# Kernel tuning notes

Hardware: AMD Instinct MI355X
Metric: run time of the kernel (lower is better)

## Reference

```python
import jax, jax.numpy as jnp
import numpy as np

D = 768
HEAD_SIZE = 64  # D / num_heads = 768 / 12

def setup_inputs() -> dict:
    key = jax.random.key(0)
    k1, k2, k3, k4 = jax.random.split(key, 4)
    ix = jax.random.normal(k1, (8, 4096, D), dtype=jnp.float32)
    # Linear(D, head_size, bias=False) weights; stored as [D, head_size] for x @ W
    scale = 1.0 / np.sqrt(D)
    Wk = jax.random.uniform(k2, (D, HEAD_SIZE), dtype=jnp.float32, minval=-scale, maxval=scale)
    Wq = jax.random.uniform(k3, (D, HEAD_SIZE), dtype=jnp.float32, minval=-scale, maxval=scale)
    Wv = jax.random.uniform(k4, (D, HEAD_SIZE), dtype=jnp.float32, minval=-scale, maxval=scale)
    return {"ix": ix, "Wk": Wk, "Wq": Wq, "Wv": Wv}

def reference(ix, Wk, Wq, Wv):
    # ix: [B, S, D]
    k = ix @ Wk  # [B, S, H]
    q = ix @ Wq  # [B, S, H]
    v = ix @ Wv  # [B, S, H]
    scale = 1.0 / jnp.sqrt(jnp.asarray(HEAD_SIZE, ix.dtype))
    wei = jnp.einsum('bsh,bth->bst', q, k) * scale  # [B, S, S]
    wei = jax.nn.softmax(wei, axis=-1)
    out = jnp.einsum('bst,bth->bsh', wei, v)  # [B, S, H]
    return out
```

## Files before the change

kernel.cpp:

```cpp
#include <hip/hip_runtime.h>
#include <hip/hip_bf16.h>

#define D_DIM 768
#define HS 64
#define SEQ 4096
#define NBATCH 8

typedef short bf8 __attribute__((ext_vector_type(8)));
typedef short bf4 __attribute__((ext_vector_type(4)));
typedef float f4 __attribute__((ext_vector_type(4)));

static __device__ __forceinline__ short f2b(float x) {
    __hip_bfloat16 h = __float2bfloat16(x);
    return __builtin_bit_cast(short, h);
}
static __device__ __forceinline__ unsigned pk2(float x, float y) {
    unsigned ux = __builtin_bit_cast(unsigned, x) + 0x8000u;
    unsigned uy = __builtin_bit_cast(unsigned, y) + 0x8000u;
    return __builtin_amdgcn_perm(uy, ux, 0x07060302u);
}

#if defined(__has_builtin)
#if __has_builtin(__builtin_amdgcn_exp2f)
#define EXP2F(x) __builtin_amdgcn_exp2f(x)
#endif
#endif
#ifndef EXP2F
#define EXP2F(x) exp2f(x)
#endif

__global__ __launch_bounds__(256) void wconv_kernel(
    const float* __restrict__ Wk, const float* __restrict__ Wq,
    const float* __restrict__ Wv, short* __restrict__ wt3)
{
    int tid = blockIdx.x * 256 + threadIdx.x;
    int mat = tid / (D_DIM * HS);
    int rem = tid - mat * (D_DIM * HS);
    int k = rem >> 6;
    int n = rem & 63;
    const float* W = (mat == 0) ? Wk : (mat == 1) ? Wq : Wv;
    float scale = (mat == 1) ? 0.18033688011112042f : 1.0f;
    int cc = mat * HS + n;
    int c = k >> 5, q = (k >> 3) & 3, e = k & 7;
    wt3[(c * 192 + cc) * 32 + q * 8 + e] = f2b(W[rem] * scale);
}

__global__ __launch_bounds__(256, 3) void proj_kernel(
    const float* __restrict__ ix, const short* __restrict__ wt3,
    short* __restrict__ qg, short* __restrict__ kg, short* __restrict__ vg)
{
    __shared__ short ixl[2][32 * 72];

    const int t = threadIdx.x;
    const int wave = t >> 6, lane = t & 63;
    const int m = lane & 15, quad = lane >> 4;
    const int m0 = blockIdx.x * 32;

    const int srow = t >> 3;
    const int skoff = (t & 7) * 8;

    f4 xr0, xr1;
    auto load_ix = [&](int c) {
        const float* px = ix + (m0 + srow) * D_DIM + c * 64 + skoff;
        xr0 = *(const f4*)px;
        xr1 = *(const f4*)(px + 4);
    };
    auto write_ix = [&](int p) {
        uint4 xw;
        xw.x = pk2(xr0[0], xr0[1]);
        xw.y = pk2(xr0[2], xr0[3]);
        xw.z = pk2(xr1[0], xr1[1]);
        xw.w = pk2(xr1[2], xr1[3]);
        *(uint4*)(&ixl[p][srow * 72 + skoff]) = xw;
    };

    const int colb = wave * 48;
    const short* wbase = wt3 + (colb + m) * 32 + quad * 8;

    bf8 wb[2][2][3];
    auto load_w = [&](int c, int buf) {
        #pragma unroll
        for (int nt = 0; nt < 3; ++nt) {
            const short* pw = wbase + ((size_t)(2 * c) * 192 + nt * 16) * 32;
            wb[buf][0][nt] = *(const bf8*)pw;
            wb[buf][1][nt] = *(const bf8*)(pw + 192 * 32);
        }
    };

    f4 acc[2][3] = {};

    load_ix(0); load_w(0, 0); write_ix(0); __syncthreads();

    #pragma unroll
    for (int c = 0; c < 12; ++c) {
        const int p = c & 1;
        if (c + 1 < 12) { load_ix(c + 1); load_w(c + 1, (c + 1) & 1); }

        bf8 a0 = *(const bf8*)(&ixl[p][m * 72 + quad * 8]);
        bf8 a1 = *(const bf8*)(&ixl[p][m * 72 + 32 + quad * 8]);
        bf8 a2 = *(const bf8*)(&ixl[p][(16 + m) * 72 + quad * 8]);
        bf8 a3 = *(const bf8*)(&ixl[p][(16 + m) * 72 + 32 + quad * 8]);

        #pragma unroll
        for (int nt = 0; nt < 3; ++nt) {
            acc[0][nt] = __builtin_amdgcn_mfma_f32_16x16x32_bf16(a0, wb[p][0][nt], acc[0][nt], 0, 0, 0);
            acc[0][nt] = __builtin_amdgcn_mfma_f32_16x16x32_bf16(a1, wb[p][1][nt], acc[0][nt], 0, 0, 0);
            acc[1][nt] = __builtin_amdgcn_mfma_f32_16x16x32_bf16(a2, wb[p][0][nt], acc[1][nt], 0, 0, 0);
            acc[1][nt] = __builtin_amdgcn_mfma_f32_16x16x32_bf16(a3, wb[p][1][nt], acc[1][nt], 0, 0, 0);
        }

        if (c + 1 < 12) { write_ix((c + 1) & 1); __syncthreads(); }
    }

    #pragma unroll
    for (int mt = 0; mt < 2; ++mt) {
        const int row = m0 + mt * 16 + quad * 4;
        #pragma unroll
        for (int nt = 0; nt < 3; ++nt) {
            const int cb = colb + nt * 16;
            short* op = (cb < 64) ? kg : (cb < 128) ? qg : vg;
            const int n = (cb & 63) + m;
            #pragma unroll
            for (int r = 0; r < 4; ++r)
                op[(row + r) * HS + n] = f2b(acc[mt][nt][r]);
        }
    }
}

__global__ __launch_bounds__(256, 2) void attn_kernel(
    const short* __restrict__ qg, const short* __restrict__ kg,
    const short* __restrict__ vg, float* __restrict__ num0,
    float* __restrict__ num1, float* __restrict__ num2,
    float* __restrict__ num3, float* __restrict__ den0,
    float* __restrict__ den1, float* __restrict__ den2,
    float* __restrict__ den3)
{
    __shared__ short kl[2][64 * 72];
    __shared__ short vl[2][64 * 64];

    const int t = threadIdx.x;
    const int wave = t >> 6, lane = t & 63;
    const int m = lane & 15, quad = lane >> 4;

    const int flat = blockIdx.x;
    const int lg = (flat & 7) * 64 + (flat >> 3);
    const int qx = lg & 15;
    const int ks = (lg >> 4) & 3;
    const int b  = lg >> 6;

    const int rbase = b * SEQ;
    const int kbase = rbase + ks * (SEQ / 4);
    const int qw = qx * 256 + wave * 64;

    float* __restrict__ nump = (ks == 0) ? num0 : (ks == 1) ? num1 : (ks == 2) ? num2 : num3;
    float* __restrict__ denp = (ks == 0) ? den0 : (ks == 1) ? den1 : (ks == 2) ? den2 : den3;

    bf8 qf[4][2];
    #pragma unroll
    for (int nq = 0; nq < 4; ++nq)
        #pragma unroll
        for (int st = 0; st < 2; ++st)
            qf[nq][st] = *(const bf8*)(qg + (rbase + qw + nq * 16 + m) * HS + st * 32 + quad * 8);

    bf8 ones;
    #pragma unroll
    for (int i = 0; i < 8; ++i) ones[i] = (short)0x3F80;

    const int srow = t >> 2, soff = (t & 3) * 16;
    const int jp = t >> 3, dg = t & 7;
    const int j0 = jp * 2;
    const int jj = j0 & 31;
    const int gj = j0 >> 5;
    const int vq = (jj >> 2) & 3;
    const int vh = (jj >> 4) & 1;
    const int vb = (jj & 3) >> 1;
    const int vcol_base = vh * 4 + 2 * vb;
    const int vchunk_l = 4 * gj + vq;

    uint4 kr0, kr1, vr0, vr1;
    auto load_chunk = [&](int c) {
        const short* pk = kg + (kbase + c * 64 + srow) * HS + soff;
        kr0 = *(const uint4*)pk; kr1 = *(const uint4*)(pk + 8);
        const short* pv = vg + (kbase + c * 64 + j0) * HS + dg * 8;
        vr0 = *(const uint4*)pv; vr1 = *(const uint4*)(pv + HS);
    };
    auto write_chunk = [&](int p) {
        *(bf8*)(&kl[p][srow * 72 + soff])     = __builtin_bit_cast(bf8, kr0);
        *(bf8*)(&kl[p][srow * 72 + soff + 8]) = __builtin_bit_cast(bf8, kr1);
        bf8 v0 = __builtin_bit_cast(bf8, vr0), v1 = __builtin_bit_cast(bf8, vr1);
        #pragma unroll
        for (int i = 0; i < 8; ++i) {
            const int d = dg * 8 + i;
            const int chunk = vchunk_l ^ (i ^ dg);
            unsigned val = (unsigned short)v0[i] | ((unsigned)(unsigned short)v1[i] << 16);
            *(unsigned*)(&vl[p][d * 64 + chunk * 8 + vcol_base]) = val;
        }
    };

    f4 o[4][4] = {};
    f4 dacc[4] = {};

    load_chunk(0); write_chunk(0); __syncthreads();

    const int NCH = SEQ / 4 / 64;
    for (int c = 0; c < NCH; ++c) {
        const int p = c & 1;
        if (c + 1 < NCH) load_chunk(c + 1);

        __builtin_amdgcn_s_setprio(1);
        #pragma unroll
        for (int g = 0; g < 2; ++g) {
            bf8 kA0 = *(const bf8*)(&kl[p][(g * 32 + m) * 72 + quad * 8]);
            bf8 kA1 = *(const bf8*)(&kl[p][(g * 32 + m) * 72 + 32 + quad * 8]);
            bf8 kB0 = *(const bf8*)(&kl[p][(g * 32 + 16 + m) * 72 + quad * 8]);
            bf8 kB1 = *(const bf8*)(&kl[p][(g * 32 + 16 + m) * 72 + 32 + quad * 8]);

            bf8 vf[4];
            #pragma unroll
            for (int dt = 0; dt < 4; ++dt) {
                const int row = dt * 16 + m;
                const int key = (m & 7) ^ (2 * dt + (m >> 3));
                const int chunk = (g * 4 + quad) ^ key;
                vf[dt] = *(const bf8*)(&vl[p][row * 64 + chunk * 8]);
            }

            #pragma unroll
            for (int nq = 0; nq < 4; ++nq) {
                f4 sa = {0.f, 0.f, 0.f, 0.f}, sb = {0.f, 0.f, 0.f, 0.f};
                sa = __builtin_amdgcn_mfma_f32_16x16x32_bf16(kA0, qf[nq][0], sa, 0, 0, 0);
                sa = __builtin_amdgcn_mfma_f32_16x16x32_bf16(kA1, qf[nq][1], sa, 0, 0, 0);
                sb = __builtin_amdgcn_mfma_f32_16x16x32_bf16(kB0, qf[nq][0], sb, 0, 0, 0);
                sb = __builtin_amdgcn_mfma_f32_16x16x32_bf16(kB1, qf[nq][1], sb, 0, 0, 0);
                float e0 = EXP2F(sa[0]), e1 = EXP2F(sa[1]), e2 = EXP2F(sa[2]), e3 = EXP2F(sa[3]);
                float e4 = EXP2F(sb[0]), e5 = EXP2F(sb[1]), e6 = EXP2F(sb[2]), e7 = EXP2F(sb[3]);
                uint4 pu;
                pu.x = pk2(e0, e1); pu.y = pk2(e2, e3);
                pu.z = pk2(e4, e5); pu.w = pk2(e6, e7);
                bf8 pf = __builtin_bit_cast(bf8, pu);
                dacc[nq] = __builtin_amdgcn_mfma_f32_16x16x32_bf16(ones, pf, dacc[nq], 0, 0, 0);
                #pragma unroll
                for (int dt = 0; dt < 4; ++dt)
                    o[nq][dt] = __builtin_amdgcn_mfma_f32_16x16x32_bf16(vf[dt], pf, o[nq][dt], 0, 0, 0);
            }
        }
        __builtin_amdgcn_s_setprio(0);

        if (c + 1 < NCH) { write_chunk((c + 1) & 1); __syncthreads(); }
    }

    #pragma unroll
    for (int nq = 0; nq < 4; ++nq) {
        const int orow = rbase + qw + nq * 16 + m;
        if (quad == 0) denp[orow] = dacc[nq][0];
        #pragma unroll
        for (int dt = 0; dt < 4; ++dt)
            *(f4*)(nump + orow * HS + dt * 16 + quad * 4) = o[nq][dt];
    }
}

__global__ __launch_bounds__(256) void reduce_kernel(
    float* __restrict__ out, const float* __restrict__ num1,
    const float* __restrict__ num2, const float* __restrict__ num3,
    const float* __restrict__ den0, const float* __restrict__ den1,
    const float* __restrict__ den2, const float* __restrict__ den3)
{
    const int gid = blockIdx.x * 256 + threadIdx.x;
    const int base = gid * 4;
    const int r = base >> 6;
    f4 n0 = *(const f4*)(out + base);
    f4 n1 = *(const f4*)(num1 + base);
    f4 n2 = *(const f4*)(num2 + base);
    f4 n3 = *(const f4*)(num3 + base);
    const float rs = 1.0f / ((den0[r] + den1[r]) + (den2[r] + den3[r]));
    f4 res;
    #pragma unroll
    for (int i = 0; i < 4; ++i) res[i] = ((n0[i] + n1[i]) + (n2[i] + n3[i])) * rs;
    *(f4*)(out + base) = res;
}

extern "C" void kernel_launch(void* const* d_in, const int* in_sizes, int n_in,
                              void* d_out, int out_size, void* d_ws, size_t ws_size,
                              hipStream_t stream) {
    const float* ix = (const float*)d_in[0];
    const float* Wk = (const float*)d_in[1];
    const float* Wq = (const float*)d_in[2];
    const float* Wv = (const float*)d_in[3];
    float* out = (float*)d_out;

    const size_t NQKV = (size_t)NBATCH * SEQ * HS;
    short* qg = (short*)d_ws;
    short* kg = qg + NQKV;
    short* vg = kg + NQKV;
    short* wt3 = vg + NQKV;
    char*  fbase = (char*)(wt3 + 24 * 192 * 32);
    float* num1 = (float*)fbase;
    float* num2 = num1 + NQKV;
    float* num3 = num2 + NQKV;
    float* den0 = num3 + NQKV;
    float* den1 = den0 + (size_t)NBATCH * SEQ;
    float* den2 = den1 + (size_t)NBATCH * SEQ;
    float* den3 = den2 + (size_t)NBATCH * SEQ;

    wconv_kernel<<<(3 * D_DIM * HS) / 256, 256, 0, stream>>>(Wk, Wq, Wv, wt3);
    proj_kernel<<<(NBATCH * SEQ) / 32, 256, 0, stream>>>(ix, wt3, qg, kg, vg);
    attn_kernel<<<512, 256, 0, stream>>>(qg, kg, vg, out, num1, num2, num3,
                                         den0, den1, den2, den3);
    reduce_kernel<<<(int)(NQKV / (256 * 4)), 256, 0, stream>>>(
        out, num1, num2, num3, den0, den1, den2, den3);
}
```

Before: 217.3 us.

## Deepen prefetch to two chunks ahead in projection and attention kernels

Both the projection and attention kernels now keep two register sets of staged global loads, so chunk c+2 is fetched while chunk c is computed. The loop is unrolled by two to alternate register sets. In the attention kernel the LDS write of the next chunk is moved between the two compute halves to overlap it with MFMA work. The aim is to hide more global-load latency, at the cost of extra VGPRs, which may reduce occupancy or cause spills under the launch bounds.

```diff
diff --git a/kernel.cpp b/kernel.cpp
--- a/kernel.cpp
+++ b/kernel.cpp
@@ -59,18 +59,18 @@
     const int srow = t >> 3;
     const int skoff = (t & 7) * 8;
 
-    f4 xr0, xr1;
-    auto load_ix = [&](int c) {
+    f4 xa0, xa1, xb0, xb1;
+    auto load_ix = [&](int c, f4& r0, f4& r1) {
         const float* px = ix + (m0 + srow) * D_DIM + c * 64 + skoff;
-        xr0 = *(const f4*)px;
-        xr1 = *(const f4*)(px + 4);
-    };
-    auto write_ix = [&](int p) {
+        r0 = *(const f4*)px;
+        r1 = *(const f4*)(px + 4);
+    };
+    auto write_ix = [&](int p, f4 r0, f4 r1) {
         uint4 xw;
-        xw.x = pk2(xr0[0], xr0[1]);
-        xw.y = pk2(xr0[2], xr0[3]);
-        xw.z = pk2(xr1[0], xr1[1]);
-        xw.w = pk2(xr1[2], xr1[3]);
+        xw.x = pk2(r0[0], r0[1]);
+        xw.y = pk2(r0[2], r0[3]);
+        xw.z = pk2(r1[0], r1[1]);
+        xw.w = pk2(r1[2], r1[3]);
         *(uint4*)(&ixl[p][srow * 72 + skoff]) = xw;
     };
 
@@ -89,18 +89,18 @@
 
     f4 acc[2][3] = {};
 
-    load_ix(0); load_w(0, 0); write_ix(0); __syncthreads();
-
-    #pragma unroll
-    for (int c = 0; c < 12; ++c) {
-        const int p = c & 1;
-        if (c + 1 < 12) { load_ix(c + 1); load_w(c + 1, (c + 1) & 1); }
-
+    load_ix(0, xa0, xa1);
+    load_w(0, 0);
+    write_ix(0, xa0, xa1);
+    load_ix(1, xb0, xb1);
+    load_w(1, 1);
+    __syncthreads();
+
+    auto mfma_block = [&](int p) {
         bf8 a0 = *(const bf8*)(&ixl[p][m * 72 + quad * 8]);
         bf8 a1 = *(const bf8*)(&ixl[p][m * 72 + 32 + quad * 8]);
         bf8 a2 = *(const bf8*)(&ixl[p][(16 + m) * 72 + quad * 8]);
         bf8 a3 = *(const bf8*)(&ixl[p][(16 + m) * 72 + 32 + quad * 8]);
-
         #pragma unroll
         for (int nt = 0; nt < 3; ++nt) {
             acc[0][nt] = __builtin_amdgcn_mfma_f32_16x16x32_bf16(a0, wb[p][0][nt], acc[0][nt], 0, 0, 0);
@@ -108,8 +108,23 @@
             acc[1][nt] = __builtin_amdgcn_mfma_f32_16x16x32_bf16(a2, wb[p][0][nt], acc[1][nt], 0, 0, 0);
             acc[1][nt] = __builtin_amdgcn_mfma_f32_16x16x32_bf16(a3, wb[p][1][nt], acc[1][nt], 0, 0, 0);
         }
-
-        if (c + 1 < 12) { write_ix((c + 1) & 1); __syncthreads(); }
+    };
+
+    for (int cc = 0; cc < 12; cc += 2) {
+        {
+            const int c = cc;
+            if (c + 2 < 12) load_ix(c + 2, xa0, xa1);
+            mfma_block(0);
+            if (c + 2 < 12) load_w(c + 2, 0);
+            if (c + 1 < 12) { write_ix(1, xb0, xb1); __syncthreads(); }
+        }
+        {
+            const int c = cc + 1;
+            if (c + 2 < 12) load_ix(c + 2, xb0, xb1);
+            mfma_block(1);
+            if (c + 2 < 12) load_w(c + 2, 1);
+            if (c + 1 < 12) { write_ix(0, xa0, xa1); __syncthreads(); }
+        }
     }
 
     #pragma unroll
@@ -155,17 +170,6 @@
     float* __restrict__ nump = (ks == 0) ? num0 : (ks == 1) ? num1 : (ks == 2) ? num2 : num3;
     float* __restrict__ denp = (ks == 0) ? den0 : (ks == 1) ? den1 : (ks == 2) ? den2 : den3;
 
-    bf8 qf[4][2];
-    #pragma unroll
-    for (int nq = 0; nq < 4; ++nq)
-        #pragma unroll
-        for (int st = 0; st < 2; ++st)
-            qf[nq][st] = *(const bf8*)(qg + (rbase + qw + nq * 16 + m) * HS + st * 32 + quad * 8);
-
-    bf8 ones;
-    #pragma unroll
-    for (int i = 0; i < 8; ++i) ones[i] = (short)0x3F80;
-
     const int srow = t >> 2, soff = (t & 3) * 16;
     const int jp = t >> 3, dg = t & 7;
     const int j0 = jp * 2;
@@ -177,17 +181,18 @@
     const int vcol_base = vh * 4 + 2 * vb;
     const int vchunk_l = 4 * gj + vq;
 
-    uint4 kr0, kr1, vr0, vr1;
-    auto load_chunk = [&](int c) {
+    uint4 kA0r, kA1r, vA0r, vA1r;
+    uint4 kB0r, kB1r, vB0r, vB1r;
+    auto load_chunk = [&](int c, uint4& k0, uint4& k1, uint4& v0, uint4& v1) {
         const short* pk = kg + (kbase + c * 64 + srow) * HS + soff;
-        kr0 = *(const uint4*)pk; kr1 = *(const uint4*)(pk + 8);
+        k0 = *(const uint4*)pk; k1 = *(const uint4*)(pk + 8);
         const short* pv = vg + (kbase + c * 64 + j0) * HS + dg * 8;
-        vr0 = *(const uint4*)pv; vr1 = *(const uint4*)(pv + HS);
-    };
-    auto write_chunk = [&](int p) {
-        *(bf8*)(&kl[p][srow * 72 + soff])     = __builtin_bit_cast(bf8, kr0);
-        *(bf8*)(&kl[p][srow * 72 + soff + 8]) = __builtin_bit_cast(bf8, kr1);
-        bf8 v0 = __builtin_bit_cast(bf8, vr0), v1 = __builtin_bit_cast(bf8, vr1);
+        v0 = *(const uint4*)pv; v1 = *(const uint4*)(pv + HS);
+    };
+    auto write_chunk = [&](int p, uint4 k0, uint4 k1, uint4 v0r, uint4 v1r) {
+        *(bf8*)(&kl[p][srow * 72 + soff])     = __builtin_bit_cast(bf8, k0);
+        *(bf8*)(&kl[p][srow * 72 + soff + 8]) = __builtin_bit_cast(bf8, k1);
+        bf8 v0 = __builtin_bit_cast(bf8, v0r), v1 = __builtin_bit_cast(bf8, v1r);
         #pragma unroll
         for (int i = 0; i < 8; ++i) {
             const int d = dg * 8 + i;
@@ -200,52 +205,84 @@
     f4 o[4][4] = {};
     f4 dacc[4] = {};
 
-    load_chunk(0); write_chunk(0); __syncthreads();
+    bf8 ones;
+    #pragma unroll
+    for (int i = 0; i < 8; ++i) ones[i] = (short)0x3F80;
+
+    load_chunk(0, kA0r, kA1r, vA0r, vA1r);
+
+    bf8 qf[4][2];
+    #pragma unroll
+    for (int nq = 0; nq < 4; ++nq)
+        #pragma unroll
+        for (int st = 0; st < 2; ++st)
+            qf[nq][st] = *(const bf8*)(qg + (rbase + qw + nq * 16 + m) * HS + st * 32 + quad * 8);
+
+    write_chunk(0, kA0r, kA1r, vA0r, vA1r);
+    load_chunk(1, kB0r, kB1r, vB0r, vB1r);
+    __syncthreads();
+
+    auto compute_g = [&](int p, int g) {
+        bf8 kA0 = *(const bf8*)(&kl[p][(g * 32 + m) * 72 + quad * 8]);
+        bf8 kA1 = *(const bf8*)(&kl[p][(g * 32 + m) * 72 + 32 + quad * 8]);
+        bf8 kB0 = *(const bf8*)(&kl[p][(g * 32 + 16 + m) * 72 + quad * 8]);
+        bf8 kB1 = *(const bf8*)(&kl[p][(g * 32 + 16 + m) * 72 + 32 + quad * 8]);
+
+        bf8 vf[4];
+        #pragma unroll
+        for (int dt = 0; dt < 4; ++dt) {
+            const int row = dt * 16 + m;
+            const int key = (m & 7) ^ (2 * dt + (m >> 3));
+            const int chunk = (g * 4 + quad) ^ key;
+            vf[dt] = *(const bf8*)(&vl[p][row * 64 + chunk * 8]);
+        }
+
+        #pragma unroll
+        for (int nq = 0; nq < 4; ++nq) {
+            f4 sa = {0.f, 0.f, 0.f, 0.f}, sb = {0.f, 0.f, 0.f, 0.f};
+            sa = __builtin_amdgcn_mfma_f32_16x16x32_bf16(kA0, qf[nq][0], sa, 0, 0, 0);
+            sa = __builtin_amdgcn_mfma_f32_16x16x32_bf16(kA1, qf[nq][1], sa, 0, 0, 0);
+            sb = __builtin_amdgcn_mfma_f32_16x16x32_bf16(kB0, qf[nq][0], sb, 0, 0, 0);
+            sb = __builtin_amdgcn_mfma_f32_16x16x32_bf16(kB1, qf[nq][1], sb, 0, 0, 0);
+            float e0 = EXP2F(sa[0]), e1 = EXP2F(sa[1]), e2 = EXP2F(sa[2]), e3 = EXP2F(sa[3]);
+            float e4 = EXP2F(sb[0]), e5 = EXP2F(sb[1]), e6 = EXP2F(sb[2]), e7 = EXP2F(sb[3]);
+            uint4 pu;
+            pu.x = pk2(e0, e1); pu.y = pk2(e2, e3);
+            pu.z = pk2(e4, e5); pu.w = pk2(e6, e7);
+            bf8 pf = __builtin_bit_cast(bf8, pu);
+            dacc[nq] = __builtin_amdgcn_mfma_f32_16x16x32_bf16(ones, pf, dacc[nq], 0, 0, 0);
+            #pragma unroll
+            for (int dt = 0; dt < 4; ++dt)
+                o[nq][dt] = __builtin_amdgcn_mfma_f32_16x16x32_bf16(vf[dt], pf, o[nq][dt], 0, 0, 0);
+        }
+    };
 
     const int NCH = SEQ / 4 / 64;
-    for (int c = 0; c < NCH; ++c) {
-        const int p = c & 1;
-        if (c + 1 < NCH) load_chunk(c + 1);
-
-        __builtin_amdgcn_s_setprio(1);
-        #pragma unroll
-        for (int g = 0; g < 2; ++g) {
-            bf8 kA0 = *(const bf8*)(&kl[p][(g * 32 + m) * 72 + quad * 8]);
-            bf8 kA1 = *(const bf8*)(&kl[p][(g * 32 + m) * 72 + 32 + quad * 8]);
-            bf8 kB0 = *(const bf8*)(&kl[p][(g * 32 + 16 + m) * 72 + quad * 8]);
-            bf8 kB1 = *(const bf8*)(&kl[p][(g * 32 + 16 + m) * 72 + 32 + quad * 8]);
-
-            bf8 vf[4];
-            #pragma unroll
-            for (int dt = 0; dt < 4; ++dt) {
-                const int row = dt * 16 + m;
-                const int key = (m & 7) ^ (2 * dt + (m >> 3));
-                const int chunk = (g * 4 + quad) ^ key;
-                vf[dt] = *(const bf8*)(&vl[p][row * 64 + chunk * 8]);
-            }
-
-            #pragma unroll
-            for (int nq = 0; nq < 4; ++nq) {
-                f4 sa = {0.f, 0.f, 0.f, 0.f}, sb = {0.f, 0.f, 0.f, 0.f};
-                sa = __builtin_amdgcn_mfma_f32_16x16x32_bf16(kA0, qf[nq][0], sa, 0, 0, 0);
-                sa = __builtin_amdgcn_mfma_f32_16x16x32_bf16(kA1, qf[nq][1], sa, 0, 0, 0);
-                sb = __builtin_amdgcn_mfma_f32_16x16x32_bf16(kB0, qf[nq][0], sb, 0, 0, 0);
-                sb = __builtin_amdgcn_mfma_f32_16x16x32_bf16(kB1, qf[nq][1], sb, 0, 0, 0);
-                float e0 = EXP2F(sa[0]), e1 = EXP2F(sa[1]), e2 = EXP2F(sa[2]), e3 = EXP2F(sa[3]);
-                float e4 = EXP2F(sb[0]), e5 = EXP2F(sb[1]), e6 = EXP2F(sb[2]), e7 = EXP2F(sb[3]);
-                uint4 pu;
-                pu.x = pk2(e0, e1); pu.y = pk2(e2, e3);
-                pu.z = pk2(e4, e5); pu.w = pk2(e6, e7);
-                bf8 pf = __builtin_bit_cast(bf8, pu);
-                dacc[nq] = __builtin_amdgcn_mfma_f32_16x16x32_bf16(ones, pf, dacc[nq], 0, 0, 0);
-                #pragma unroll
-                for (int dt = 0; dt < 4; ++dt)
-                    o[nq][dt] = __builtin_amdgcn_mfma_f32_16x16x32_bf16(vf[dt], pf, o[nq][dt], 0, 0, 0);
-            }
-        }
-        __builtin_amdgcn_s_setprio(0);
-
-        if (c + 1 < NCH) { write_chunk((c + 1) & 1); __syncthreads(); }
+    for (int cc = 0; cc < NCH; cc += 2) {
+        {
+            const int c = cc;
+            if (c + 2 < NCH) load_chunk(c + 2, kA0r, kA1r, vA0r, vA1r);
+            __builtin_amdgcn_s_setprio(1);
+            compute_g(0, 0);
+            __builtin_amdgcn_s_setprio(0);
+            if (c + 1 < NCH) write_chunk(1, kB0r, kB1r, vB0r, vB1r);
+            __builtin_amdgcn_s_setprio(1);
+            compute_g(0, 1);
+            __builtin_amdgcn_s_setprio(0);
+            if (c + 1 < NCH) __syncthreads();
+        }
+        {
+            const int c = cc + 1;
+            if (c + 2 < NCH) load_chunk(c + 2, kB0r, kB1r, vB0r, vB1r);
+            __builtin_amdgcn_s_setprio(1);
+            compute_g(1, 0);
+            __builtin_amdgcn_s_setprio(0);
+            if (c + 1 < NCH) write_chunk(0, kA0r, kA1r, vA0r, vA1r);
+            __builtin_amdgcn_s_setprio(1);
+            compute_g(1, 1);
+            __builtin_amdgcn_s_setprio(0);
+            if (c + 1 < NCH) __syncthreads();
+        }
     }
 
     #pragma unroll
```

After: 216.5 us. About the same (-0.4%).
